# Performance work log

Hardware: AMD Instinct MI355X
Metric: run time of the kernel (lower is better)

Reference implementation:

```python
import jax, jax.numpy as jnp
import numpy as np

NUM_NODES = 50000
NUM_RELATIONS = 16
NUM_EDGES = 800000
HIDDEN = 64
NUM_CLASSES = 16


def setup_inputs() -> dict:
    key = jax.random.key(0)
    ks = jax.random.split(key, 8)
    edge_index = jax.random.randint(ks[0], (2, NUM_EDGES), 0, NUM_NODES, dtype=jnp.int32)
    edge_type = jax.random.randint(ks[1], (NUM_EDGES,), 0, NUM_RELATIONS, dtype=jnp.int32)
    node_emb = jax.random.normal(ks[2], (NUM_NODES, HIDDEN), dtype=jnp.float32) * 0.1
    W1 = jax.random.normal(ks[3], (NUM_RELATIONS, HIDDEN, HIDDEN), dtype=jnp.float32) * 0.1
    root1 = jax.random.normal(ks[4], (HIDDEN, HIDDEN), dtype=jnp.float32) * 0.1
    b1 = jnp.zeros((HIDDEN,), dtype=jnp.float32)
    W2 = jax.random.normal(ks[5], (NUM_RELATIONS, HIDDEN, NUM_CLASSES), dtype=jnp.float32) * 0.1
    root2 = jax.random.normal(ks[6], (HIDDEN, NUM_CLASSES), dtype=jnp.float32) * 0.1
    b2 = jnp.zeros((NUM_CLASSES,), dtype=jnp.float32)
    return {"edge_index": edge_index, "edge_type": edge_type, "node_emb": node_emb,
            "W1": W1, "root1": root1, "b1": b1, "W2": W2, "root2": root2, "b2": b2}


def rgcn_conv(x, src, dst, edge_type, W, root, bias, num_nodes):
    # PyG RGCNConv (aggr='mean', root_weight=True, bias=True, num_bases=None):
    # per relation r: transform all nodes, gather at src, scatter-MEAN at dst
    # (mean over edges of that relation per target node); sum over relations;
    # then add root transform and bias.
    out_dim = W.shape[-1]

    def body(acc, rw):
        W_r, r = rw
        h = x @ W_r                                   # [N, out]
        mask = (edge_type == r).astype(x.dtype)       # [E]
        msg = h[src] * mask[:, None]                  # [E, out]
        summed = jax.ops.segment_sum(msg, dst, num_segments=num_nodes)  # [N, out]
        cnt = jax.ops.segment_sum(mask, dst, num_segments=num_nodes)    # [N]
        mean = jnp.where(cnt[:, None] > 0, summed / jnp.maximum(cnt, 1.0)[:, None], 0.0)
        return acc + mean, None

    acc0 = jnp.zeros((num_nodes, out_dim), dtype=x.dtype)
    agg, _ = jax.lax.scan(body, acc0, (W, jnp.arange(W.shape[0])))
    return agg + x @ root + bias


def reference(edge_index, edge_type, node_emb, W1, root1, b1, W2, root2, b2):
    src, dst = edge_index[0], edge_index[1]
    n = node_emb.shape[0]
    x = rgcn_conv(node_emb, src, dst, edge_type, W1, root1, b1, n)
    x = jax.nn.relu(x)  # dropout p=0.0 -> identity
    x = rgcn_conv(x, src, dst, edge_type, W2, root2, b2, n)
    return x
```

## Files before the change

kernel.cpp:

```cpp
#include <hip/hip_runtime.h>
#include <hip/hip_bf16.h>

#define N_NODES 50000
#define NREL 16
#define HID 64
#define NCLS 16
#define NTILES 3125
#define NBKT (N_NODES * NREL)
#define SB 2048
#define NSB ((NBKT + SB - 1) / SB)
#define TBLK 196
#define NGRP 6

typedef __attribute__((ext_vector_type(8))) short bf16x8;
typedef __attribute__((ext_vector_type(4))) float f32x4;

static __device__ __forceinline__ unsigned short f2bf(float f) {
    __hip_bfloat16 h = __float2bfloat16(f);
    return *reinterpret_cast<unsigned short*>(&h);
}
static __device__ __forceinline__ float bf2f(unsigned short u) {
    __hip_bfloat16 h;
    *reinterpret_cast<unsigned short*>(&h) = u;
    return __bfloat162float(h);
}


__global__ __launch_bounds__(256) void rank_k(const int* __restrict__ dstp,
                                              const int* __restrict__ et,
                                              int* __restrict__ bcnt,
                                              int* __restrict__ rank, int E) {
    int i = blockIdx.x * 256 + threadIdx.x;
    if (i < E) {
        int b = dstp[i] * NREL + et[i];
        rank[i] = atomicAdd(&bcnt[b], 1);
    }
}

__global__ __launch_bounds__(256) void scan1_k(const int* __restrict__ bcnt,
                                               int* __restrict__ bsum) {
    int b = blockIdx.x, t = threadIdx.x;
    int base = b * SB + t * 8;
    int s = 0;
#pragma unroll
    for (int j = 0; j < 8; ++j)
        if (base + j < NBKT) s += bcnt[base + j];
#pragma unroll
    for (int off = 1; off < 64; off <<= 1) s += __shfl_xor(s, off, 64);
    __shared__ int ws[4];
    if ((t & 63) == 0) ws[t >> 6] = s;
    __syncthreads();
    if (t == 0) bsum[b] = ws[0] + ws[1] + ws[2] + ws[3];
}

__global__ __launch_bounds__(512) void scan2_k(int* __restrict__ bsum,
                                               int* __restrict__ rstart, int E) {
    __shared__ int ts[512];
    int t = threadIdx.x;
    int v = (t < NSB) ? bsum[t] : 0;
    ts[t] = v;
    __syncthreads();
    int acc = v;
    for (int off = 1; off < 512; off <<= 1) {
        int u = (t >= off) ? ts[t - off] : 0;
        __syncthreads();
        acc += u;
        ts[t] = acc;
        __syncthreads();
    }
    if (t < NSB) bsum[t] = acc - v;
    if (t == 0) rstart[NBKT] = E;
}

__global__ __launch_bounds__(256) void scan3_k(int* __restrict__ bcnt,
                                               const int* __restrict__ bsum) {
    int b = blockIdx.x, t = threadIdx.x;
    int base = b * SB + t * 8;
    int a[8];
    int s = 0;
#pragma unroll
    for (int j = 0; j < 8; ++j) {
        a[j] = (base + j < NBKT) ? bcnt[base + j] : 0;
        s += a[j];
    }
    __shared__ int ts[256];
    ts[t] = s;
    __syncthreads();
    int acc = s;
    for (int off = 1; off < 256; off <<= 1) {
        int u = (t >= off) ? ts[t - off] : 0;
        __syncthreads();
        acc += u;
        ts[t] = acc;
        __syncthreads();
    }
    int run = bsum[b] + (acc - s);
#pragma unroll
    for (int j = 0; j < 8; ++j) {
        if (base + j < NBKT) bcnt[base + j] = run;
        run += a[j];
    }
}

__global__ __launch_bounds__(256) void scat_k(const int* __restrict__ srcp,
                                              const int* __restrict__ dstp,
                                              const int* __restrict__ et,
                                              const int* __restrict__ rank,
                                              const int* __restrict__ rstart,
                                              int2* __restrict__ sedge,
                                              unsigned char* __restrict__ used,
                                              int E) {
    int i = blockIdx.x * 256 + threadIdx.x;
    if (i < E) {
        int r = et[i];
        int s = srcp[i];
        int b = dstp[i] * NREL + r;
        int lo = rstart[b], hi = rstart[b + 1];
        int p = lo + rank[i];
        float inv = 1.0f / (float)(hi - lo);
        sedge[p] = make_int2(s | (r << 16), __float_as_int(inv));
        used[r * N_NODES + s] = 1;
    }
}

__global__ __launch_bounds__(256) void cvtw_k(const float* __restrict__ W1,
                                              const float* __restrict__ root1,
                                              const float* __restrict__ W2,
                                              const float* __restrict__ root2,
                                              ushort* __restrict__ WbT1,
                                              ushort* __restrict__ WbT2) {
    int i = blockIdx.x * 256 + threadIdx.x;
    if (i < 17 * HID * HID) {
        int t = i >> 12;
        int rem = i & 4095;
        int n = rem >> 6, k = rem & 63;
        float v = (t < 16) ? W1[(size_t)t * HID * HID + k * HID + n]
                           : root1[k * HID + n];
        WbT1[i] = f2bf(v);
    } else {
        int j = i - 17 * HID * HID;
        if (j < 17 * NCLS * HID) {
            int t = j >> 10;
            int rem = j & 1023;
            int n = rem >> 6, k = rem & 63;
            float v = (t < 16) ? W2[(size_t)t * HID * NCLS + k * NCLS + n]
                               : root2[k * NCLS + n];
            WbT2[j] = f2bf(v);
        }
    }
}

__global__ __launch_bounds__(256) void trans1_k(const float* __restrict__ x,
                                                const ushort* __restrict__ WbT1,
                                                const float* __restrict__ b1,
                                                const unsigned char* __restrict__ used,
                                                ushort* __restrict__ H1,
                                                ushort* __restrict__ X1m) {
    int grp = blockIdx.x / TBLK;
    int blkin = blockIdx.x - grp * TBLK;
    int wave = threadIdx.x >> 6;
    int lane = threadIdx.x & 63;
    int mr = lane & 15;
    int kq = lane >> 4;
    int tileBase = blkin * 16 + wave * 4;

    bf16x8 a0[4] = {}, a1[4] = {};
#pragma unroll
    for (int q = 0; q < 4; ++q) {
        if (tileBase + q < NTILES) {
            const float* xr = x + (size_t)((tileBase + q) * 16 + mr) * HID + kq * 8;
            float4 f0 = *(const float4*)(xr);
            float4 f1 = *(const float4*)(xr + 4);
            float4 f2 = *(const float4*)(xr + 32);
            float4 f3 = *(const float4*)(xr + 36);
            bf16x8 t0v, t1v;
            t0v[0] = (short)f2bf(f0.x); t0v[1] = (short)f2bf(f0.y);
            t0v[2] = (short)f2bf(f0.z); t0v[3] = (short)f2bf(f0.w);
            t0v[4] = (short)f2bf(f1.x); t0v[5] = (short)f2bf(f1.y);
            t0v[6] = (short)f2bf(f1.z); t0v[7] = (short)f2bf(f1.w);
            t1v[0] = (short)f2bf(f2.x); t1v[1] = (short)f2bf(f2.y);
            t1v[2] = (short)f2bf(f2.z); t1v[3] = (short)f2bf(f2.w);
            t1v[4] = (short)f2bf(f3.x); t1v[5] = (short)f2bf(f3.y);
            t1v[6] = (short)f2bf(f3.z); t1v[7] = (short)f2bf(f3.w);
            a0[q] = t0v;
            a1[q] = t1v;
        }
    }

    int t0 = grp * 3;
    int t1 = (grp == NGRP - 1) ? 17 : (t0 + 3);

    for (int t = t0; t < t1; ++t) {
        const ushort* wt = WbT1 + (size_t)t * HID * HID + mr * HID + kq * 8;
        bf16x8 b0[4], bv[4];
#pragma unroll
        for (int nt = 0; nt < 4; ++nt) {
            b0[nt] = *(const bf16x8*)(wt + nt * 1024);
            bv[nt] = *(const bf16x8*)(wt + nt * 1024 + 32);
        }
#pragma unroll
        for (int q = 0; q < 4; ++q) {
            if (tileBase + q >= NTILES) continue;
            int n0 = (tileBase + q) * 16;
            f32x4 acc[4];
#pragma unroll
            for (int nt = 0; nt < 4; ++nt) {
                f32x4 c = {0.f, 0.f, 0.f, 0.f};
                c = __builtin_amdgcn_mfma_f32_16x16x32_bf16(a0[q], b0[nt], c, 0, 0, 0);
                c = __builtin_amdgcn_mfma_f32_16x16x32_bf16(a1[q], bv[nt], c, 0, 0, 0);
                acc[nt] = c;
            }
            if (t < 16) {
                uchar4 uf = *(const uchar4*)(used + (size_t)t * N_NODES + n0 + kq * 4);
                ushort* Ht = H1 + (size_t)t * N_NODES * HID;
#pragma unroll
                for (int r = 0; r < 4; ++r) {
                    unsigned char f = (r == 0) ? uf.x : (r == 1) ? uf.y
                                     : (r == 2) ? uf.z : uf.w;
                    if (f) {
                        int node = n0 + kq * 4 + r;
                        ushort4 o;
                        o.x = f2bf(acc[0][r]); o.y = f2bf(acc[1][r]);
                        o.z = f2bf(acc[2][r]); o.w = f2bf(acc[3][r]);
                        *(ushort4*)(Ht + (size_t)node * HID + mr * 4) = o;
                    }
                }
            } else {
#pragma unroll
                for (int nt = 0; nt < 4; ++nt) {
                    float bias = b1[nt * 16 + mr];
#pragma unroll
                    for (int r = 0; r < 4; ++r) {
                        int node = n0 + kq * 4 + r;
                        X1m[(size_t)node * HID + nt * 16 + mr] =
                            f2bf(acc[nt][r] + bias);
                    }
                }
            }
        }
    }
}

__global__ __launch_bounds__(256) void edge1_k(const int2* __restrict__ sedge,
                                               const int* __restrict__ rstart,
                                               const ushort* __restrict__ H1,
                                               ushort* __restrict__ X1m) {
    int wid = __builtin_amdgcn_readfirstlane((blockIdx.x * 256 + threadIdx.x) >> 6);
    int lane = threadIdx.x & 63;
    if (wid >= N_NODES) return;
    int col = (lane & 3) * 16 + (lane >> 2);
    int lo = rstart[wid << 4], hi = rstart[(wid + 1) << 4];
    float accA = bf2f(X1m[(size_t)wid * HID + col]);
    float accB = 0.0f;
    int e = lo;
    for (; e + 8 <= hi; e += 8) {
        int2 m0 = sedge[e],     m1 = sedge[e + 1], m2 = sedge[e + 2], m3 = sedge[e + 3];
        int2 m4 = sedge[e + 4], m5 = sedge[e + 5], m6 = sedge[e + 6], m7 = sedge[e + 7];
        float v0 = bf2f(H1[((size_t)(m0.x >> 16) * N_NODES + (m0.x & 0xFFFF)) * HID + lane]);
        float v1 = bf2f(H1[((size_t)(m1.x >> 16) * N_NODES + (m1.x & 0xFFFF)) * HID + lane]);
        float v2 = bf2f(H1[((size_t)(m2.x >> 16) * N_NODES + (m2.x & 0xFFFF)) * HID + lane]);
        float v3 = bf2f(H1[((size_t)(m3.x >> 16) * N_NODES + (m3.x & 0xFFFF)) * HID + lane]);
        float v4 = bf2f(H1[((size_t)(m4.x >> 16) * N_NODES + (m4.x & 0xFFFF)) * HID + lane]);
        float v5 = bf2f(H1[((size_t)(m5.x >> 16) * N_NODES + (m5.x & 0xFFFF)) * HID + lane]);
        float v6 = bf2f(H1[((size_t)(m6.x >> 16) * N_NODES + (m6.x & 0xFFFF)) * HID + lane]);
        float v7 = bf2f(H1[((size_t)(m7.x >> 16) * N_NODES + (m7.x & 0xFFFF)) * HID + lane]);
        accA = fmaf(__int_as_float(m0.y), v0, accA);
        accB = fmaf(__int_as_float(m1.y), v1, accB);
        accA = fmaf(__int_as_float(m2.y), v2, accA);
        accB = fmaf(__int_as_float(m3.y), v3, accB);
        accA = fmaf(__int_as_float(m4.y), v4, accA);
        accB = fmaf(__int_as_float(m5.y), v5, accB);
        accA = fmaf(__int_as_float(m6.y), v6, accA);
        accB = fmaf(__int_as_float(m7.y), v7, accB);
    }
    for (; e + 4 <= hi; e += 4) {
        int2 m0 = sedge[e], m1 = sedge[e + 1], m2 = sedge[e + 2], m3 = sedge[e + 3];
        float v0 = bf2f(H1[((size_t)(m0.x >> 16) * N_NODES + (m0.x & 0xFFFF)) * HID + lane]);
        float v1 = bf2f(H1[((size_t)(m1.x >> 16) * N_NODES + (m1.x & 0xFFFF)) * HID + lane]);
        float v2 = bf2f(H1[((size_t)(m2.x >> 16) * N_NODES + (m2.x & 0xFFFF)) * HID + lane]);
        float v3 = bf2f(H1[((size_t)(m3.x >> 16) * N_NODES + (m3.x & 0xFFFF)) * HID + lane]);
        accA = fmaf(__int_as_float(m0.y), v0, accA);
        accB = fmaf(__int_as_float(m1.y), v1, accB);
        accA = fmaf(__int_as_float(m2.y), v2, accA);
        accB = fmaf(__int_as_float(m3.y), v3, accB);
    }
    for (; e < hi; ++e) {
        int2 m = sedge[e];
        float v = bf2f(H1[((size_t)(m.x >> 16) * N_NODES + (m.x & 0xFFFF)) * HID + lane]);
        accA = fmaf(__int_as_float(m.y), v, accA);
    }
    float acc = accA + accB;
    X1m[(size_t)wid * HID + col] = f2bf(fmaxf(acc, 0.f));
}

__global__ __launch_bounds__(256) void trans2_k(const ushort* __restrict__ X1m,
                                                const ushort* __restrict__ WbT2,
                                                const float* __restrict__ b2,
                                                const unsigned char* __restrict__ used,
                                                ushort* __restrict__ H2,
                                                float* __restrict__ out) {
    int grp = blockIdx.x / TBLK;
    int blkin = blockIdx.x - grp * TBLK;
    int wave = threadIdx.x >> 6;
    int lane = threadIdx.x & 63;
    int mr = lane & 15, kq = lane >> 4;
    int tileBase = blkin * 16 + wave * 4;

    bf16x8 a0[4] = {}, a1[4] = {};
#pragma unroll
    for (int q = 0; q < 4; ++q) {
        if (tileBase + q < NTILES) {
            const bf16x8* arow =
                (const bf16x8*)(X1m + (size_t)((tileBase + q) * 16 + mr) * HID + kq * 8);
            a0[q] = arow[0];
            a1[q] = arow[4];
        }
    }

    int t0 = grp * 3;
    int t1 = (grp == NGRP - 1) ? 17 : (t0 + 3);

    for (int t = t0; t < t1; ++t) {
        const ushort* wt = WbT2 + (size_t)t * NCLS * HID + mr * HID + kq * 8;
        bf16x8 b0 = *(const bf16x8*)(wt);
        bf16x8 bv = *(const bf16x8*)(wt + 32);
#pragma unroll
        for (int q = 0; q < 4; ++q) {
            if (tileBase + q >= NTILES) continue;
            int n0 = (tileBase + q) * 16;
            f32x4 c = {0.f, 0.f, 0.f, 0.f};
            c = __builtin_amdgcn_mfma_f32_16x16x32_bf16(a0[q], b0, c, 0, 0, 0);
            c = __builtin_amdgcn_mfma_f32_16x16x32_bf16(a1[q], bv, c, 0, 0, 0);
            if (t < 16) {
                uchar4 uf = *(const uchar4*)(used + (size_t)t * N_NODES + n0 + kq * 4);
                ushort* Ht = H2 + (size_t)t * N_NODES * NCLS;
#pragma unroll
                for (int r = 0; r < 4; ++r) {
                    unsigned char f = (r == 0) ? uf.x : (r == 1) ? uf.y
                                     : (r == 2) ? uf.z : uf.w;
                    if (f) {
                        int node = n0 + kq * 4 + r;
                        Ht[(size_t)node * NCLS + mr] = f2bf(c[r]);
                    }
                }
            } else {
                float bias = b2[mr];
#pragma unroll
                for (int r = 0; r < 4; ++r) {
                    int node = n0 + kq * 4 + r;
                    out[(size_t)node * NCLS + mr] = c[r] + bias;
                }
            }
        }
    }
}

__global__ __launch_bounds__(256) void edge2_k(const int2* __restrict__ sedge,
                                               const int* __restrict__ rstart,
                                               const ushort* __restrict__ H2,
                                               float* __restrict__ out) {
    int wid = __builtin_amdgcn_readfirstlane((blockIdx.x * 256 + threadIdx.x) >> 6);
    int lane = threadIdx.x & 63;
    int g = lane >> 4, c = lane & 15;
    int d0 = wid * 4 + g;
    if (d0 < N_NODES) {
        int lo = rstart[d0 << 4], hi = rstart[(d0 + 1) << 4];
        float accA = out[(size_t)d0 * NCLS + c];
        float accB = 0.0f;
        int e = lo;
        for (; e + 4 <= hi; e += 4) {
            int2 m0 = sedge[e], m1 = sedge[e + 1], m2 = sedge[e + 2], m3 = sedge[e + 3];
            float v0 = bf2f(H2[((size_t)(m0.x >> 16) * N_NODES + (m0.x & 0xFFFF)) * NCLS + c]);
            float v1 = bf2f(H2[((size_t)(m1.x >> 16) * N_NODES + (m1.x & 0xFFFF)) * NCLS + c]);
            float v2 = bf2f(H2[((size_t)(m2.x >> 16) * N_NODES + (m2.x & 0xFFFF)) * NCLS + c]);
            float v3 = bf2f(H2[((size_t)(m3.x >> 16) * N_NODES + (m3.x & 0xFFFF)) * NCLS + c]);
            accA = fmaf(__int_as_float(m0.y), v0, accA);
            accB = fmaf(__int_as_float(m1.y), v1, accB);
            accA = fmaf(__int_as_float(m2.y), v2, accA);
            accB = fmaf(__int_as_float(m3.y), v3, accB);
        }
        for (; e < hi; ++e) {
            int2 m = sedge[e];
            float v = bf2f(H2[((size_t)(m.x >> 16) * N_NODES + (m.x & 0xFFFF)) * NCLS + c]);
            accA = fmaf(__int_as_float(m.y), v, accA);
        }
        out[(size_t)d0 * NCLS + c] = accA + accB;
    }
}

extern "C" void kernel_launch(void* const* d_in, const int* in_sizes, int n_in,
                              void* d_out, int out_size, void* d_ws, size_t ws_size,
                              hipStream_t stream) {
    const int* ei    = (const int*)d_in[0];
    const int* et    = (const int*)d_in[1];
    const float* x   = (const float*)d_in[2];
    const float* W1  = (const float*)d_in[3];
    const float* r1  = (const float*)d_in[4];
    const float* b1  = (const float*)d_in[5];
    const float* W2  = (const float*)d_in[6];
    const float* r2  = (const float*)d_in[7];
    const float* b2  = (const float*)d_in[8];
    float* out = (float*)d_out;

    int E = in_sizes[0] / 2;
    const int* srcp = ei;
    const int* dstp = ei + E;

    int*   bcnt   = (int*)d_ws;
    unsigned char* used = (unsigned char*)(bcnt + (NBKT + 20));
    int*   rank   = (int*)(used + NBKT);
    int*   bsum   = rank + E;
    int2*  sedge  = (int2*)(bsum + 512);
    ushort* WbT1  = (ushort*)(sedge + E);
    ushort* WbT2  = WbT1 + 17 * HID * HID;
    ushort* H1    = WbT2 + 17 * NCLS * HID;
    ushort* H2    = H1 + (size_t)NREL * N_NODES * HID;
    ushort* X1m   = H2 + (size_t)NREL * N_NODES * NCLS;
    int*   rstart = bcnt;

    hipMemsetAsync(bcnt, 0, (NBKT + 20) * sizeof(int) + NBKT, stream);

    int eb = (E + 255) / 256;
    int cvtThreads = 17 * HID * HID + 17 * NCLS * HID;

    cvtw_k<<<(cvtThreads + 255) / 256, 256, 0, stream>>>(W1, r1, W2, r2, WbT1, WbT2);
    rank_k<<<eb, 256, 0, stream>>>(dstp, et, bcnt, rank, E);
    scan1_k<<<NSB, 256, 0, stream>>>(bcnt, bsum);
    scan2_k<<<1, 512, 0, stream>>>(bsum, rstart, E);
    scan3_k<<<NSB, 256, 0, stream>>>(bcnt, bsum);
    scat_k<<<eb, 256, 0, stream>>>(srcp, dstp, et, rank, rstart, sedge, used, E);

    trans1_k<<<NGRP * TBLK, 256, 0, stream>>>(x, WbT1, b1, used, H1, X1m);
    edge1_k<<<(N_NODES + 3) / 4, 256, 0, stream>>>(sedge, rstart, H1, X1m);
    trans2_k<<<NGRP * TBLK, 256, 0, stream>>>(X1m, WbT2, b2, used, H2, out);
    edge2_k<<<(N_NODES / 4 + 3) / 4, 256, 0, stream>>>(sedge, rstart, H2, out);
}
```

Before: 273.5 us.

## Aggregate-then-transform: fuse per-relation mean gather with MFMA transform per tile

Reorders each layer from transform-all-nodes-per-relation then gather into gather-then-transform. Each block first builds per-relation mean-aggregated inputs (64-wide bf16 for 16 relations plus the root row) in swizzled LDS for 32 destination nodes, then multiplies them by the stacked weights with MFMA. This removes the large H1/H2 intermediates (16×N×64 bf16) and the used-mask pass, shrinking memory traffic to gathers of raw bf16 features. The cost is lower parallelism in the gather (one 8-lane group per node, serial loop over edges) and a large LDS footprint per block.

```diff
diff --git a/kernel.cpp b/kernel.cpp
--- a/kernel.cpp
+++ b/kernel.cpp
@@ -5,12 +5,14 @@
 #define NREL 16
 #define HID 64
 #define NCLS 16
-#define NTILES 3125
 #define NBKT (N_NODES * NREL)
 #define SB 2048
 #define NSB ((NBKT + SB - 1) / SB)
-#define TBLK 196
-#define NGRP 6
+#define TILE 32
+#define NTB ((N_NODES + TILE - 1) / TILE)
+#define XCHUNKS (N_NODES * HID / 8)
+#define W1N (17 * HID * HID)
+#define W2N (17 * NCLS * HID)
 
 typedef __attribute__((ext_vector_type(8))) short bf16x8;
 typedef __attribute__((ext_vector_type(4))) float f32x4;
@@ -25,6 +27,43 @@
     return __bfloat162float(h);
 }
 
+
+__global__ __launch_bounds__(256) void cvt_k(const float* __restrict__ x,
+                                             const float* __restrict__ W1,
+                                             const float* __restrict__ root1,
+                                             const float* __restrict__ W2,
+                                             const float* __restrict__ root2,
+                                             ushort* __restrict__ xb,
+                                             ushort* __restrict__ WbT1,
+                                             ushort* __restrict__ WbT2) {
+    int i = blockIdx.x * 256 + threadIdx.x;
+    if (i < XCHUNKS) {
+        float4 f0 = *(const float4*)(x + (size_t)i * 8);
+        float4 f1 = *(const float4*)(x + (size_t)i * 8 + 4);
+        bf16x8 o;
+        o[0] = (short)f2bf(f0.x); o[1] = (short)f2bf(f0.y);
+        o[2] = (short)f2bf(f0.z); o[3] = (short)f2bf(f0.w);
+        o[4] = (short)f2bf(f1.x); o[5] = (short)f2bf(f1.y);
+        o[6] = (short)f2bf(f1.z); o[7] = (short)f2bf(f1.w);
+        *(bf16x8*)(xb + (size_t)i * 8) = o;
+    } else {
+        int j = i - XCHUNKS;
+        if (j < W1N) {
+            int t = j >> 12, rem = j & 4095, n = rem >> 6, k = rem & 63;
+            float v = (t < 16) ? W1[(size_t)t * HID * HID + k * HID + n]
+                               : root1[k * HID + n];
+            WbT1[j] = f2bf(v);
+        } else {
+            int m = j - W1N;
+            if (m < W2N) {
+                int t = m >> 10, rem = m & 1023, n = rem >> 6, k = rem & 63;
+                float v = (t < 16) ? W2[(size_t)t * HID * NCLS + k * NCLS + n]
+                                   : root2[k * NCLS + n];
+                WbT2[m] = f2bf(v);
+            }
+        }
+    }
+}
 
 __global__ __launch_bounds__(256) void rank_k(const int* __restrict__ dstp,
                                               const int* __restrict__ et,
@@ -107,284 +146,182 @@
                                               const int* __restrict__ et,
                                               const int* __restrict__ rank,
                                               const int* __restrict__ rstart,
-                                              int2* __restrict__ sedge,
-                                              unsigned char* __restrict__ used,
-                                              int E) {
+                                              int* __restrict__ sedge, int E) {
     int i = blockIdx.x * 256 + threadIdx.x;
     if (i < E) {
-        int r = et[i];
-        int s = srcp[i];
-        int b = dstp[i] * NREL + r;
-        int lo = rstart[b], hi = rstart[b + 1];
-        int p = lo + rank[i];
-        float inv = 1.0f / (float)(hi - lo);
-        sedge[p] = make_int2(s | (r << 16), __float_as_int(inv));
-        used[r * N_NODES + s] = 1;
-    }
-}
-
-__global__ __launch_bounds__(256) void cvtw_k(const float* __restrict__ W1,
-                                              const float* __restrict__ root1,
-                                              const float* __restrict__ W2,
-                                              const float* __restrict__ root2,
-                                              ushort* __restrict__ WbT1,
-                                              ushort* __restrict__ WbT2) {
-    int i = blockIdx.x * 256 + threadIdx.x;
-    if (i < 17 * HID * HID) {
-        int t = i >> 12;
-        int rem = i & 4095;
-        int n = rem >> 6, k = rem & 63;
-        float v = (t < 16) ? W1[(size_t)t * HID * HID + k * HID + n]
-                           : root1[k * HID + n];
-        WbT1[i] = f2bf(v);
-    } else {
-        int j = i - 17 * HID * HID;
-        if (j < 17 * NCLS * HID) {
-            int t = j >> 10;
-            int rem = j & 1023;
-            int n = rem >> 6, k = rem & 63;
-            float v = (t < 16) ? W2[(size_t)t * HID * NCLS + k * NCLS + n]
-                               : root2[k * NCLS + n];
-            WbT2[j] = f2bf(v);
+        int b = dstp[i] * NREL + et[i];
+        sedge[rstart[b] + rank[i]] = srcp[i];
+    }
+}
+
+
+__global__ __launch_bounds__(256) void fuse1_k(const ushort* __restrict__ xb,
+                                               const int* __restrict__ sedge,
+                                               const int* __restrict__ rstart,
+                                               const ushort* __restrict__ WbT1,
+                                               const float* __restrict__ b1,
+                                               ushort* __restrict__ X1b) {
+    __shared__ bf16x8 Abuf[17 * TILE * 8];
+    char* Ab = (char*)Abuf;
+    int tid = threadIdx.x;
+    int dst0 = blockIdx.x * TILE;
+
+    {
+        int row = tid >> 3, ch = tid & 7;
+        int node = dst0 + row;
+        bf16x8 v = {0, 0, 0, 0, 0, 0, 0, 0};
+        if (node < N_NODES) v = *(const bf16x8*)(xb + (size_t)node * HID + ch * 8);
+        int addr = (((16 * TILE + row) << 7) + (ch << 4)) ^ ((row & 7) << 4);
+        *(bf16x8*)(Ab + addr) = v;
+    }
+
+    {
+        int g = tid >> 3, l8 = tid & 7;
+        int node = dst0 + g;
+        bool valid = node < N_NODES;
+        const ushort* xcol = xb + l8 * 8;
+        int lo = valid ? rstart[node * NREL] : 0;
+        for (int r = 0; r < NREL; ++r) {
+            int hi = valid ? rstart[node * NREL + r + 1] : 0;
+            float acc[8] = {0.f, 0.f, 0.f, 0.f, 0.f, 0.f, 0.f, 0.f};
+            int cnt = hi - lo;
+            for (int e = lo; e < hi; ++e) {
+                int src = sedge[e];
+                bf16x8 v = *(const bf16x8*)(xcol + (size_t)src * HID);
+#pragma unroll
+                for (int j = 0; j < 8; ++j) acc[j] += bf2f((unsigned short)v[j]);
+            }
+            float s = (cnt > 0) ? 1.0f / (float)cnt : 0.0f;
+            bf16x8 o;
+#pragma unroll
+            for (int j = 0; j < 8; ++j) o[j] = (short)f2bf(acc[j] * s);
+            int addr = (((r * TILE + g) << 7) + (l8 << 4)) ^ ((g & 7) << 4);
+            *(bf16x8*)(Ab + addr) = o;
+            lo = hi;
         }
     }
-}
-
-__global__ __launch_bounds__(256) void trans1_k(const float* __restrict__ x,
-                                                const ushort* __restrict__ WbT1,
-                                                const float* __restrict__ b1,
-                                                const unsigned char* __restrict__ used,
-                                                ushort* __restrict__ H1,
-                                                ushort* __restrict__ X1m) {
-    int grp = blockIdx.x / TBLK;
-    int blkin = blockIdx.x - grp * TBLK;
-    int wave = threadIdx.x >> 6;
-    int lane = threadIdx.x & 63;
-    int mr = lane & 15;
-    int kq = lane >> 4;
-    int tileBase = blkin * 16 + wave * 4;
-
-    bf16x8 a0[4] = {}, a1[4] = {};
-#pragma unroll
-    for (int q = 0; q < 4; ++q) {
-        if (tileBase + q < NTILES) {
-            const float* xr = x + (size_t)((tileBase + q) * 16 + mr) * HID + kq * 8;
-            float4 f0 = *(const float4*)(xr);
-            float4 f1 = *(const float4*)(xr + 4);
-            float4 f2 = *(const float4*)(xr + 32);
-            float4 f3 = *(const float4*)(xr + 36);
-            bf16x8 t0v, t1v;
-            t0v[0] = (short)f2bf(f0.x); t0v[1] = (short)f2bf(f0.y);
-            t0v[2] = (short)f2bf(f0.z); t0v[3] = (short)f2bf(f0.w);
-            t0v[4] = (short)f2bf(f1.x); t0v[5] = (short)f2bf(f1.y);
-            t0v[6] = (short)f2bf(f1.z); t0v[7] = (short)f2bf(f1.w);
-            t1v[0] = (short)f2bf(f2.x); t1v[1] = (short)f2bf(f2.y);
-            t1v[2] = (short)f2bf(f2.z); t1v[3] = (short)f2bf(f2.w);
-            t1v[4] = (short)f2bf(f3.x); t1v[5] = (short)f2bf(f3.y);
-            t1v[6] = (short)f2bf(f3.z); t1v[7] = (short)f2bf(f3.w);
-            a0[q] = t0v;
-            a1[q] = t1v;
+    __syncthreads();
+
+    int wave = tid >> 6, lane = tid & 63;
+    int mr = lane & 15, kq = lane >> 4;
+    f32x4 c0 = {0.f, 0.f, 0.f, 0.f}, c1 = {0.f, 0.f, 0.f, 0.f};
+    const ushort* wb = WbT1 + (wave * 16 + mr) * HID + kq * 8;
+    int sw = (mr & 7) << 4;
+    int a00o = ((mr << 7) + (kq << 4)) ^ sw;
+    int a01o = ((mr << 7) + 64 + (kq << 4)) ^ sw;
+    int a10o = (((16 + mr) << 7) + (kq << 4)) ^ sw;
+    int a11o = (((16 + mr) << 7) + 64 + (kq << 4)) ^ sw;
+    for (int t = 0; t < 17; ++t) {
+        bf16x8 bk0 = *(const bf16x8*)(wb + t * 4096);
+        bf16x8 bk1 = *(const bf16x8*)(wb + t * 4096 + 32);
+        const char* At = Ab + t * (TILE * 128);
+        bf16x8 a00 = *(const bf16x8*)(At + a00o);
+        bf16x8 a01 = *(const bf16x8*)(At + a01o);
+        bf16x8 a10 = *(const bf16x8*)(At + a10o);
+        bf16x8 a11 = *(const bf16x8*)(At + a11o);
+        c0 = __builtin_amdgcn_mfma_f32_16x16x32_bf16(a00, bk0, c0, 0, 0, 0);
+        c0 = __builtin_amdgcn_mfma_f32_16x16x32_bf16(a01, bk1, c0, 0, 0, 0);
+        c1 = __builtin_amdgcn_mfma_f32_16x16x32_bf16(a10, bk0, c1, 0, 0, 0);
+        c1 = __builtin_amdgcn_mfma_f32_16x16x32_bf16(a11, bk1, c1, 0, 0, 0);
+    }
+    float bias = b1[wave * 16 + mr];
+    int col = wave * 16 + mr;
+#pragma unroll
+    for (int j = 0; j < 4; ++j) {
+        int r0 = dst0 + kq * 4 + j;
+        if (r0 < N_NODES)
+            X1b[(size_t)r0 * HID + col] = f2bf(fmaxf(c0[j] + bias, 0.f));
+        int r1 = r0 + 16;
+        if (r1 < N_NODES)
+            X1b[(size_t)r1 * HID + col] = f2bf(fmaxf(c1[j] + bias, 0.f));
+    }
+}
+
+__global__ __launch_bounds__(256) void fuse2_k(const ushort* __restrict__ X1b,
+                                               const int* __restrict__ sedge,
+                                               const int* __restrict__ rstart,
+                                               const ushort* __restrict__ WbT2,
+                                               const float* __restrict__ b2,
+                                               float* __restrict__ out) {
+    __shared__ bf16x8 Abuf[17 * TILE * 8];
+    __shared__ float P[4 * TILE * NCLS];
+    char* Ab = (char*)Abuf;
+    int tid = threadIdx.x;
+    int dst0 = blockIdx.x * TILE;
+
+    {
+        int row = tid >> 3, ch = tid & 7;
+        int node = dst0 + row;
+        bf16x8 v = {0, 0, 0, 0, 0, 0, 0, 0};
+        if (node < N_NODES) v = *(const bf16x8*)(X1b + (size_t)node * HID + ch * 8);
+        int addr = (((16 * TILE + row) << 7) + (ch << 4)) ^ ((row & 7) << 4);
+        *(bf16x8*)(Ab + addr) = v;
+    }
+    {
+        int g = tid >> 3, l8 = tid & 7;
+        int node = dst0 + g;
+        bool valid = node < N_NODES;
+        const ushort* xcol = X1b + l8 * 8;
+        int lo = valid ? rstart[node * NREL] : 0;
+        for (int r = 0; r < NREL; ++r) {
+            int hi = valid ? rstart[node * NREL + r + 1] : 0;
+            float acc[8] = {0.f, 0.f, 0.f, 0.f, 0.f, 0.f, 0.f, 0.f};
+            int cnt = hi - lo;
+            for (int e = lo; e < hi; ++e) {
+                int src = sedge[e];
+                bf16x8 v = *(const bf16x8*)(xcol + (size_t)src * HID);
+#pragma unroll
+                for (int j = 0; j < 8; ++j) acc[j] += bf2f((unsigned short)v[j]);
+            }
+            float s = (cnt > 0) ? 1.0f / (float)cnt : 0.0f;
+            bf16x8 o;
+#pragma unroll
+            for (int j = 0; j < 8; ++j) o[j] = (short)f2bf(acc[j] * s);
+            int addr = (((r * TILE + g) << 7) + (l8 << 4)) ^ ((g & 7) << 4);
+            *(bf16x8*)(Ab + addr) = o;
+            lo = hi;
         }
     }
-
-    int t0 = grp * 3;
-    int t1 = (grp == NGRP - 1) ? 17 : (t0 + 3);
-
-    for (int t = t0; t < t1; ++t) {
-        const ushort* wt = WbT1 + (size_t)t * HID * HID + mr * HID + kq * 8;
-        bf16x8 b0[4], bv[4];
-#pragma unroll
-        for (int nt = 0; nt < 4; ++nt) {
-            b0[nt] = *(const bf16x8*)(wt + nt * 1024);
-            bv[nt] = *(const bf16x8*)(wt + nt * 1024 + 32);
-        }
-#pragma unroll
-        for (int q = 0; q < 4; ++q) {
-            if (tileBase + q >= NTILES) continue;
-            int n0 = (tileBase + q) * 16;
-            f32x4 acc[4];
-#pragma unroll
-            for (int nt = 0; nt < 4; ++nt) {
-                f32x4 c = {0.f, 0.f, 0.f, 0.f};
-                c = __builtin_amdgcn_mfma_f32_16x16x32_bf16(a0[q], b0[nt], c, 0, 0, 0);
-                c = __builtin_amdgcn_mfma_f32_16x16x32_bf16(a1[q], bv[nt], c, 0, 0, 0);
-                acc[nt] = c;
-            }
-            if (t < 16) {
-                uchar4 uf = *(const uchar4*)(used + (size_t)t * N_NODES + n0 + kq * 4);
-                ushort* Ht = H1 + (size_t)t * N_NODES * HID;
-#pragma unroll
-                for (int r = 0; r < 4; ++r) {
-                    unsigned char f = (r == 0) ? uf.x : (r == 1) ? uf.y
-                                     : (r == 2) ? uf.z : uf.w;
-                    if (f) {
-                        int node = n0 + kq * 4 + r;
-                        ushort4 o;
-                        o.x = f2bf(acc[0][r]); o.y = f2bf(acc[1][r]);
-                        o.z = f2bf(acc[2][r]); o.w = f2bf(acc[3][r]);
-                        *(ushort4*)(Ht + (size_t)node * HID + mr * 4) = o;
-                    }
-                }
-            } else {
-#pragma unroll
-                for (int nt = 0; nt < 4; ++nt) {
-                    float bias = b1[nt * 16 + mr];
-#pragma unroll
-                    for (int r = 0; r < 4; ++r) {
-                        int node = n0 + kq * 4 + r;
-                        X1m[(size_t)node * HID + nt * 16 + mr] =
-                            f2bf(acc[nt][r] + bias);
-                    }
-                }
-            }
-        }
-    }
-}
-
-__global__ __launch_bounds__(256) void edge1_k(const int2* __restrict__ sedge,
-                                               const int* __restrict__ rstart,
-                                               const ushort* __restrict__ H1,
-                                               ushort* __restrict__ X1m) {
-    int wid = __builtin_amdgcn_readfirstlane((blockIdx.x * 256 + threadIdx.x) >> 6);
-    int lane = threadIdx.x & 63;
-    if (wid >= N_NODES) return;
-    int col = (lane & 3) * 16 + (lane >> 2);
-    int lo = rstart[wid << 4], hi = rstart[(wid + 1) << 4];
-    float accA = bf2f(X1m[(size_t)wid * HID + col]);
-    float accB = 0.0f;
-    int e = lo;
-    for (; e + 8 <= hi; e += 8) {
-        int2 m0 = sedge[e],     m1 = sedge[e + 1], m2 = sedge[e + 2], m3 = sedge[e + 3];
-        int2 m4 = sedge[e + 4], m5 = sedge[e + 5], m6 = sedge[e + 6], m7 = sedge[e + 7];
-        float v0 = bf2f(H1[((size_t)(m0.x >> 16) * N_NODES + (m0.x & 0xFFFF)) * HID + lane]);
-        float v1 = bf2f(H1[((size_t)(m1.x >> 16) * N_NODES + (m1.x & 0xFFFF)) * HID + lane]);
-        float v2 = bf2f(H1[((size_t)(m2.x >> 16) * N_NODES + (m2.x & 0xFFFF)) * HID + lane]);
-        float v3 = bf2f(H1[((size_t)(m3.x >> 16) * N_NODES + (m3.x & 0xFFFF)) * HID + lane]);
-        float v4 = bf2f(H1[((size_t)(m4.x >> 16) * N_NODES + (m4.x & 0xFFFF)) * HID + lane]);
-        float v5 = bf2f(H1[((size_t)(m5.x >> 16) * N_NODES + (m5.x & 0xFFFF)) * HID + lane]);
-        float v6 = bf2f(H1[((size_t)(m6.x >> 16) * N_NODES + (m6.x & 0xFFFF)) * HID + lane]);
-        float v7 = bf2f(H1[((size_t)(m7.x >> 16) * N_NODES + (m7.x & 0xFFFF)) * HID + lane]);
-        accA = fmaf(__int_as_float(m0.y), v0, accA);
-        accB = fmaf(__int_as_float(m1.y), v1, accB);
-        accA = fmaf(__int_as_float(m2.y), v2, accA);
-        accB = fmaf(__int_as_float(m3.y), v3, accB);
-        accA = fmaf(__int_as_float(m4.y), v4, accA);
-        accB = fmaf(__int_as_float(m5.y), v5, accB);
-        accA = fmaf(__int_as_float(m6.y), v6, accA);
-        accB = fmaf(__int_as_float(m7.y), v7, accB);
-    }
-    for (; e + 4 <= hi; e += 4) {
-        int2 m0 = sedge[e], m1 = sedge[e + 1], m2 = sedge[e + 2], m3 = sedge[e + 3];
-        float v0 = bf2f(H1[((size_t)(m0.x >> 16) * N_NODES + (m0.x & 0xFFFF)) * HID + lane]);
-        float v1 = bf2f(H1[((size_t)(m1.x >> 16) * N_NODES + (m1.x & 0xFFFF)) * HID + lane]);
-        float v2 = bf2f(H1[((size_t)(m2.x >> 16) * N_NODES + (m2.x & 0xFFFF)) * HID + lane]);
-        float v3 = bf2f(H1[((size_t)(m3.x >> 16) * N_NODES + (m3.x & 0xFFFF)) * HID + lane]);
-        accA = fmaf(__int_as_float(m0.y), v0, accA);
-        accB = fmaf(__int_as_float(m1.y), v1, accB);
-        accA = fmaf(__int_as_float(m2.y), v2, accA);
-        accB = fmaf(__int_as_float(m3.y), v3, accB);
-    }
-    for (; e < hi; ++e) {
-        int2 m = sedge[e];
-        float v = bf2f(H1[((size_t)(m.x >> 16) * N_NODES + (m.x & 0xFFFF)) * HID + lane]);
-        accA = fmaf(__int_as_float(m.y), v, accA);
-    }
-    float acc = accA + accB;
-    X1m[(size_t)wid * HID + col] = f2bf(fmaxf(acc, 0.f));
-}
-
-__global__ __launch_bounds__(256) void trans2_k(const ushort* __restrict__ X1m,
-                                                const ushort* __restrict__ WbT2,
-                                                const float* __restrict__ b2,
-                                                const unsigned char* __restrict__ used,
-                                                ushort* __restrict__ H2,
-                                                float* __restrict__ out) {
-    int grp = blockIdx.x / TBLK;
-    int blkin = blockIdx.x - grp * TBLK;
-    int wave = threadIdx.x >> 6;
-    int lane = threadIdx.x & 63;
+    __syncthreads();
+
+    int wave = tid >> 6, lane = tid & 63;
     int mr = lane & 15, kq = lane >> 4;
-    int tileBase = blkin * 16 + wave * 4;
-
-    bf16x8 a0[4] = {}, a1[4] = {};
-#pragma unroll
-    for (int q = 0; q < 4; ++q) {
-        if (tileBase + q < NTILES) {
-            const bf16x8* arow =
-                (const bf16x8*)(X1m + (size_t)((tileBase + q) * 16 + mr) * HID + kq * 8);
-            a0[q] = arow[0];
-            a1[q] = arow[4];
-        }
-    }
-
-    int t0 = grp * 3;
-    int t1 = (grp == NGRP - 1) ? 17 : (t0 + 3);
-
-    for (int t = t0; t < t1; ++t) {
-        const ushort* wt = WbT2 + (size_t)t * NCLS * HID + mr * HID + kq * 8;
-        bf16x8 b0 = *(const bf16x8*)(wt);
-        bf16x8 bv = *(const bf16x8*)(wt + 32);
-#pragma unroll
-        for (int q = 0; q < 4; ++q) {
-            if (tileBase + q >= NTILES) continue;
-            int n0 = (tileBase + q) * 16;
-            f32x4 c = {0.f, 0.f, 0.f, 0.f};
-            c = __builtin_amdgcn_mfma_f32_16x16x32_bf16(a0[q], b0, c, 0, 0, 0);
-            c = __builtin_amdgcn_mfma_f32_16x16x32_bf16(a1[q], bv, c, 0, 0, 0);
-            if (t < 16) {
-                uchar4 uf = *(const uchar4*)(used + (size_t)t * N_NODES + n0 + kq * 4);
-                ushort* Ht = H2 + (size_t)t * N_NODES * NCLS;
-#pragma unroll
-                for (int r = 0; r < 4; ++r) {
-                    unsigned char f = (r == 0) ? uf.x : (r == 1) ? uf.y
-                                     : (r == 2) ? uf.z : uf.w;
-                    if (f) {
-                        int node = n0 + kq * 4 + r;
-                        Ht[(size_t)node * NCLS + mr] = f2bf(c[r]);
-                    }
-                }
-            } else {
-                float bias = b2[mr];
-#pragma unroll
-                for (int r = 0; r < 4; ++r) {
-                    int node = n0 + kq * 4 + r;
-                    out[(size_t)node * NCLS + mr] = c[r] + bias;
-                }
-            }
-        }
-    }
-}
-
-__global__ __launch_bounds__(256) void edge2_k(const int2* __restrict__ sedge,
-                                               const int* __restrict__ rstart,
-                                               const ushort* __restrict__ H2,
-                                               float* __restrict__ out) {
-    int wid = __builtin_amdgcn_readfirstlane((blockIdx.x * 256 + threadIdx.x) >> 6);
-    int lane = threadIdx.x & 63;
-    int g = lane >> 4, c = lane & 15;
-    int d0 = wid * 4 + g;
-    if (d0 < N_NODES) {
-        int lo = rstart[d0 << 4], hi = rstart[(d0 + 1) << 4];
-        float accA = out[(size_t)d0 * NCLS + c];
-        float accB = 0.0f;
-        int e = lo;
-        for (; e + 4 <= hi; e += 4) {
-            int2 m0 = sedge[e], m1 = sedge[e + 1], m2 = sedge[e + 2], m3 = sedge[e + 3];
-            float v0 = bf2f(H2[((size_t)(m0.x >> 16) * N_NODES + (m0.x & 0xFFFF)) * NCLS + c]);
-            float v1 = bf2f(H2[((size_t)(m1.x >> 16) * N_NODES + (m1.x & 0xFFFF)) * NCLS + c]);
-            float v2 = bf2f(H2[((size_t)(m2.x >> 16) * N_NODES + (m2.x & 0xFFFF)) * NCLS + c]);
-            float v3 = bf2f(H2[((size_t)(m3.x >> 16) * N_NODES + (m3.x & 0xFFFF)) * NCLS + c]);
-            accA = fmaf(__int_as_float(m0.y), v0, accA);
-            accB = fmaf(__int_as_float(m1.y), v1, accB);
-            accA = fmaf(__int_as_float(m2.y), v2, accA);
-            accB = fmaf(__int_as_float(m3.y), v3, accB);
-        }
-        for (; e < hi; ++e) {
-            int2 m = sedge[e];
-            float v = bf2f(H2[((size_t)(m.x >> 16) * N_NODES + (m.x & 0xFFFF)) * NCLS + c]);
-            accA = fmaf(__int_as_float(m.y), v, accA);
-        }
-        out[(size_t)d0 * NCLS + c] = accA + accB;
+    f32x4 c0 = {0.f, 0.f, 0.f, 0.f}, c1 = {0.f, 0.f, 0.f, 0.f};
+    const ushort* wb = WbT2 + mr * HID + kq * 8;
+    int sw = (mr & 7) << 4;
+    int a00o = ((mr << 7) + (kq << 4)) ^ sw;
+    int a01o = ((mr << 7) + 64 + (kq << 4)) ^ sw;
+    int a10o = (((16 + mr) << 7) + (kq << 4)) ^ sw;
+    int a11o = (((16 + mr) << 7) + 64 + (kq << 4)) ^ sw;
+    for (int t = wave; t < 17; t += 4) {
+        bf16x8 bk0 = *(const bf16x8*)(wb + t * 1024);
+        bf16x8 bk1 = *(const bf16x8*)(wb + t * 1024 + 32);
+        const char* At = Ab + t * (TILE * 128);
+        bf16x8 a00 = *(const bf16x8*)(At + a00o);
+        bf16x8 a01 = *(const bf16x8*)(At + a01o);
+        bf16x8 a10 = *(const bf16x8*)(At + a10o);
+        bf16x8 a11 = *(const bf16x8*)(At + a11o);
+        c0 = __builtin_amdgcn_mfma_f32_16x16x32_bf16(a00, bk0, c0, 0, 0, 0);
+        c0 = __builtin_amdgcn_mfma_f32_16x16x32_bf16(a01, bk1, c0, 0, 0, 0);
+        c1 = __builtin_amdgcn_mfma_f32_16x16x32_bf16(a10, bk0, c1, 0, 0, 0);
+        c1 = __builtin_amdgcn_mfma_f32_16x16x32_bf16(a11, bk1, c1, 0, 0, 0);
+    }
+    float* Pw = P + wave * (TILE * NCLS);
+#pragma unroll
+    for (int j = 0; j < 4; ++j) {
+        Pw[(kq * 4 + j) * NCLS + mr] = c0[j];
+        Pw[(16 + kq * 4 + j) * NCLS + mr] = c1[j];
+    }
+    __syncthreads();
+
+    int idx = tid * 2;
+    int row = idx >> 4, c = idx & 15;
+    float s0 = P[idx] + P[512 + idx] + P[1024 + idx] + P[1536 + idx] + b2[c];
+    float s1 = P[idx + 1] + P[512 + idx + 1] + P[1024 + idx + 1] +
+               P[1536 + idx + 1] + b2[c + 1];
+    if (dst0 + row < N_NODES) {
+        float2 o = make_float2(s0, s1);
+        *(float2*)(out + (size_t)(dst0 + row) * NCLS + c) = o;
     }
 }
 
@@ -406,32 +343,28 @@
     const int* srcp = ei;
     const int* dstp = ei + E;
 
-    int*   bcnt   = (int*)d_ws;
-    unsigned char* used = (unsigned char*)(bcnt + (NBKT + 20));
-    int*   rank   = (int*)(used + NBKT);
-    int*   bsum   = rank + E;
-    int2*  sedge  = (int2*)(bsum + 512);
+    int*    bcnt  = (int*)d_ws;
+    int*    rank  = bcnt + (NBKT + 20);
+    int*    bsum  = rank + E;
+    int*    sedge = bsum + 512;
     ushort* WbT1  = (ushort*)(sedge + E);
-    ushort* WbT2  = WbT1 + 17 * HID * HID;
-    ushort* H1    = WbT2 + 17 * NCLS * HID;
-    ushort* H2    = H1 + (size_t)NREL * N_NODES * HID;
-    ushort* X1m   = H2 + (size_t)NREL * N_NODES * NCLS;
-    int*   rstart = bcnt;
-
-    hipMemsetAsync(bcnt, 0, (NBKT + 20) * sizeof(int) + NBKT, stream);
+    ushort* WbT2  = WbT1 + W1N;
+    ushort* xb    = WbT2 + W2N;
+    ushort* X1b   = xb + (size_t)N_NODES * HID;
+    int*    rstart = bcnt;
+
+    hipMemsetAsync(bcnt, 0, (NBKT + 20) * sizeof(int), stream);
 
     int eb = (E + 255) / 256;
-    int cvtThreads = 17 * HID * HID + 17 * NCLS * HID;
-
-    cvtw_k<<<(cvtThreads + 255) / 256, 256, 0, stream>>>(W1, r1, W2, r2, WbT1, WbT2);
+    int cvtThreads = XCHUNKS + W1N + W2N;
+
+    cvt_k<<<(cvtThreads + 255) / 256, 256, 0, stream>>>(x, W1, r1, W2, r2, xb, WbT1, WbT2);
     rank_k<<<eb, 256, 0, stream>>>(dstp, et, bcnt, rank, E);
     scan1_k<<<NSB, 256, 0, stream>>>(bcnt, bsum);
     scan2_k<<<1, 512, 0, stream>>>(bsum, rstart, E);
     scan3_k<<<NSB, 256, 0, stream>>>(bcnt, bsum);
-    scat_k<<<eb, 256, 0, stream>>>(srcp, dstp, et, rank, rstart, sedge, used, E);
-
-    trans1_k<<<NGRP * TBLK, 256, 0, stream>>>(x, WbT1, b1, used, H1, X1m);
-    edge1_k<<<(N_NODES + 3) / 4, 256, 0, stream>>>(sedge, rstart, H1, X1m);
-    trans2_k<<<NGRP * TBLK, 256, 0, stream>>>(X1m, WbT2, b2, used, H2, out);
-    edge2_k<<<(N_NODES / 4 + 3) / 4, 256, 0, stream>>>(sedge, rstart, H2, out);
-}
+    scat_k<<<eb, 256, 0, stream>>>(srcp, dstp, et, rank, rstart, sedge, E);
+
+    fuse1_k<<<NTB, 256, 0, stream>>>(xb, sedge, rstart, WbT1, b1, X1b);
+    fuse2_k<<<NTB, 256, 0, stream>>>(X1b, sedge, rstart, WbT2, b2, out);
+}
```

Result: slower. 412.8 us (+50.9%).
